# Optimization experiments

Measured on AMD Instinct MI355X. Metric: run time of the kernel, lower is better.

Reference implementation:

```python
import jax, jax.numpy as jnp
import numpy as np

N_NODES = 50000
N_EDGES = 800000
N_REL = 3
N_GRAPHS = 500
EMB = 128
IN_DIM = EMB * 3
HID = 256
N_CLASS = 10
N_SHAPE, N_COLOR, MAX_POS = 8, 8, 128


def rgcn_layer(h, src, dst, etype, W, root, b):
    """PyG RGCNConv with default aggr='mean':
    out[v] = sum_r mean_{(j->v) in E_r} h[j] @ W[r] + h[v] @ root + b
    Aggregate raw features per (dst, relation) bucket, then apply relation matmuls.
    """
    N, R = h.shape[0], W.shape[0]
    seg = dst * R + etype  # combined (node, relation) segment id
    sums = jax.ops.segment_sum(h[src], seg, num_segments=N * R)          # (N*R, d)
    cnt = jax.ops.segment_sum(jnp.ones(seg.shape, h.dtype), seg, num_segments=N * R)
    mean = (sums / jnp.maximum(cnt, 1.0)[:, None]).reshape(N, R, -1)     # (N, R, d)
    return jnp.einsum('nrd,rdh->nh', mean, W) + h @ root + b


def setup_inputs() -> dict:
    key = jax.random.key(0)
    ks = jax.random.split(key, 20)
    f32 = jnp.float32
    inp = {
        's': jax.random.randint(ks[0], (N_NODES,), 0, N_SHAPE),
        'c': jax.random.randint(ks[1], (N_NODES,), 0, N_COLOR),
        'p': jax.random.randint(ks[2], (N_NODES,), 0, MAX_POS),
        'edge_index': jax.random.randint(ks[3], (2, N_EDGES), 0, N_NODES),
        'edge_type': jax.random.randint(ks[4], (N_EDGES,), 0, N_REL),
        'batch': jnp.sort(jax.random.randint(ks[5], (N_NODES,), 0, N_GRAPHS)),
        'shape_emb': jax.random.normal(ks[6], (N_SHAPE, EMB), f32),
        'color_emb': jax.random.normal(ks[7], (N_COLOR, EMB), f32),
        'pos_emb': jax.random.normal(ks[8], (MAX_POS, EMB), f32),
        'W1': jax.random.normal(ks[9], (N_REL, IN_DIM, HID), f32) / np.sqrt(IN_DIM),
        'root1': jax.random.normal(ks[10], (IN_DIM, HID), f32) / np.sqrt(IN_DIM),
        'b1': jnp.zeros((HID,), f32),
        'W2': jax.random.normal(ks[11], (N_REL, HID, HID), f32) / np.sqrt(HID),
        'root2': jax.random.normal(ks[12], (HID, HID), f32) / np.sqrt(HID),
        'b2': jnp.zeros((HID,), f32),
        'lin_w': jax.random.normal(ks[13], (HID, N_CLASS), f32) / np.sqrt(HID),
        'lin_b': jnp.zeros((N_CLASS,), f32),
    }
    return inp


def reference(s, c, p, edge_index, edge_type, batch,
              shape_emb, color_emb, pos_emb,
              W1, root1, b1, W2, root2, b2, lin_w, lin_b):
    src, dst = edge_index[0], edge_index[1]
    h = jnp.concatenate([shape_emb[s], color_emb[c], pos_emb[p]], axis=-1)  # (N, 3*emb)
    h = jax.nn.relu(rgcn_layer(h, src, dst, edge_type, W1, root1, b1))
    h = jax.nn.relu(rgcn_layer(h, src, dst, edge_type, W2, root2, b2))
    # global_mean_pool over graphs
    gsum = jax.ops.segment_sum(h, batch, num_segments=N_GRAPHS)
    gcnt = jax.ops.segment_sum(jnp.ones((h.shape[0],), h.dtype), batch, num_segments=N_GRAPHS)
    pooled = gsum / jnp.maximum(gcnt, 1.0)[:, None]
    return pooled @ lin_w + lin_b
```

## Files before the change

kernel.cpp:

```cpp
#include <hip/hip_runtime.h>
#include <hip/hip_bf16.h>

#define NN 50000
#define NE 800000
#define NR 3
#define NG 500
#define NB (NN * NR)
#define NCLS 10
#define NCMB 8192
#define CHUNK 2048
#define NBLK ((NB + CHUNK - 1) / CHUNK)

#define P1_COMBO   196
#define P1_ZCNT    586
#define P1_ZPOOL   502
#define P1_TAB     576
#define P1_WF      1024
#define P1_TOTAL   (P1_COMBO + P1_ZCNT + P1_ZPOOL + P1_TAB + P1_WF)
#define P2_CNT     3125
#define P2_TB      768
#define P2_TOTAL   (P2_CNT + P2_TB)

#define L1_DPB     64
#define L1_HS      776
#define L1_BLOCKS  ((NN + L1_DPB - 1) / L1_DPB)

typedef __hip_bfloat16 bf16;
typedef __attribute__((ext_vector_type(8))) short short8;
typedef __attribute__((ext_vector_type(4))) short shortx4;
typedef __attribute__((ext_vector_type(4))) float floatx4;

static __device__ __forceinline__ float b2f(bf16 x) { return __bfloat162float(x); }
static __device__ __forceinline__ bf16  f2b(float x) { return __float2bfloat16(x); }
static __device__ __forceinline__ float bs2f(short x) {
    return __bfloat162float(*reinterpret_cast<const bf16*>(&x));
}
static __device__ __forceinline__ short f2bs(float x) {
    bf16 b = __float2bfloat16(x);
    return *reinterpret_cast<const short*>(&b);
}
static __device__ __forceinline__ int rfl(int x) {
    return __builtin_amdgcn_readfirstlane(x);
}

__global__ __launch_bounds__(256) void prep1(const int* __restrict__ s,
                                             const int* __restrict__ c,
                                             const int* __restrict__ p,
                                             const float* __restrict__ se,
                                             const float* __restrict__ ce,
                                             const float* __restrict__ pe,
                                             const float* __restrict__ W1,
                                             const float* __restrict__ root1,
                                             const float* __restrict__ W2,
                                             const float* __restrict__ root2,
                                             int* __restrict__ combo,
                                             unsigned* __restrict__ cnt,
                                             unsigned* __restrict__ poolz,
                                             float* __restrict__ tab,
                                             bf16* __restrict__ Wf) {
    int b = blockIdx.x, t = threadIdx.x;
    if (b < P1_COMBO) {
        int n = b * 256 + t;
        if (n < NN) combo[n] = (s[n] << 10) | (c[n] << 7) | p[n];
        return;
    }
    b -= P1_COMBO;
    if (b < P1_ZCNT) {
        int i = b * 256 + t;
        if (i < NB) cnt[i] = 0u;
        return;
    }
    b -= P1_ZCNT;
    if (b < P1_ZPOOL) {
        int i = b * 256 + t;
        if (i < NG * 256 + NG) poolz[i] = 0u;
        return;
    }
    b -= P1_ZPOOL;
    if (b < P1_TAB) {
        int r = b / 144, row = b % 144;
        const float* A; int segk;
        if (row < 8)       { A = se + row * 128;        segk = 0; }
        else if (row < 16) { A = ce + (row - 8) * 128;  segk = 128; }
        else               { A = pe + (row - 16) * 128; segk = 256; }
        const float* W = (r < 3) ? (W1 + (size_t)r * 384 * 256) : root1;
        float acc = 0.f;
        for (int k = 0; k < 128; ++k)
            acc += A[k] * W[(size_t)(segk + k) * 256 + t];
        tab[((size_t)r * 144 + row) * 256 + t] = acc;
        return;
    }
    b -= P1_TAB;
    {
        int idx = b * 256 + t;
        int j     = idx & 7;
        int lane  = (idx >> 3) & 63;
        int ni    = (idx >> 9) & 3;
        int chunk = (idx >> 11) & 31;
        int colblk = idx >> 16;
        int col = colblk * 64 + ni * 16 + (lane & 15);
        int k   = chunk * 32 + (lane >> 4) * 8 + j;
        float v = (k < 768) ? W2[((size_t)(k >> 8) * 256 + (k & 255)) * 256 + col]
                            : root2[(size_t)(k - 768) * 256 + col];
        Wf[idx] = f2b(v);
    }
}

__global__ __launch_bounds__(256) void prep2(const int* __restrict__ ei,
                                             const int* __restrict__ et,
                                             int* __restrict__ cnt,
                                             const float* __restrict__ tab,
                                             const float* __restrict__ b1,
                                             bf16* __restrict__ tb2) {
    int b = blockIdx.x, t = threadIdx.x;
    if (b < P2_CNT) {
        int e = b * 256 + t;
        if (e < NE) atomicAdd(&cnt[ei[NE + e] * NR + et[e]], 1);
        return;
    }
    b -= P2_CNT;
    if (b < 256) {
        int r = b >> 6, sc = b & 63, si = sc >> 3, ci = sc & 7;
        float v = tab[((size_t)r * 144 + si) * 256 + t]
                + tab[((size_t)r * 144 + 8 + ci) * 256 + t];
        if (r == 3) v += b1[t];
        tb2[(size_t)b * 256 + t] = f2b(v);
    } else {
        int bb = b - 256;
        int r = bb >> 7, pi = bb & 127;
        tb2[(size_t)(256 + bb) * 256 + t] =
            f2b(tab[((size_t)r * 144 + 16 + pi) * 256 + t]);
    }
}

__global__ __launch_bounds__(256) void prep3(const bf16* __restrict__ tb2,
                                             bf16* __restrict__ tbf) {
    int idx = blockIdx.x * 256 + threadIdx.x;
    int j = idx & 7, lane = (idx >> 3) & 63, ni = (idx >> 9) & 3;
    int rest = idx >> 11;
    int chunk = rest % 24, colblk = rest / 24;
    int col = colblk * 64 + ni * 16 + (lane & 15);
    int k   = chunk * 32 + (lane >> 4) * 8 + j;
    tbf[idx] = tb2[(size_t)k * 256 + col];
}

__global__ __launch_bounds__(256) void scan_block_sums(const int* __restrict__ cnt,
                                                       int* __restrict__ bsum) {
    __shared__ int sm[256];
    int b = blockIdx.x, t = threadIdx.x;
    int base = b * CHUNK + t * 8, s = 0;
#pragma unroll
    for (int j = 0; j < 8; ++j) { int i = base + j; if (i < NB) s += cnt[i]; }
    sm[t] = s; __syncthreads();
    for (int st = 128; st; st >>= 1) { if (t < st) sm[t] += sm[t + st]; __syncthreads(); }
    if (!t) bsum[b] = sm[0];
}

__global__ __launch_bounds__(256) void scan_write(const int* __restrict__ cnt,
                                                  const int* __restrict__ bsum,
                                                  int* __restrict__ off,
                                                  int* __restrict__ cursor) {
    int b = blockIdx.x, t = threadIdx.x;
    int bbase = 0;
    for (int i = 0; i < b; ++i) bbase += bsum[i];
    if (b == 0 && t == 0) {
        int tot = 0;
        for (int i = 0; i < NBLK; ++i) tot += bsum[i];
        off[NB] = tot;
    }
    int base = b * CHUNK + t * 8;
    int v[8], ts = 0;
#pragma unroll
    for (int j = 0; j < 8; ++j) { int i = base + j; v[j] = (i < NB) ? cnt[i] : 0; ts += v[j]; }
    int lane = t & 63, wv = t >> 6;
    int incl = ts;
    for (int d = 1; d < 64; d <<= 1) {
        int o = __shfl_up(incl, d, 64);
        if (lane >= d) incl += o;
    }
    __shared__ int wsum[4];
    if (lane == 63) wsum[wv] = incl;
    __syncthreads();
    int wbase = 0;
    for (int w = 0; w < wv; ++w) wbase += wsum[w];
    int run = bbase + wbase + incl - ts;
#pragma unroll
    for (int j = 0; j < 8; ++j) {
        int i = base + j;
        if (i < NB) { off[i] = run; cursor[i] = run; }
        run += v[j];
    }
}

__global__ __launch_bounds__(256) void scatter_edges(const int* __restrict__ ei,
                                                     const int* __restrict__ et,
                                                     const int* __restrict__ combo,
                                                     int* __restrict__ cursor,
                                                     unsigned* __restrict__ esc) {
    int e = blockIdx.x * 256 + threadIdx.x;
    if (e >= NE) return;
    int b = ei[NE + e] * NR + et[e];
    int pos = atomicAdd(&cursor[b], 1);
    int s = ei[e];
    esc[pos] = ((unsigned)s << 13) | (unsigned)combo[s];
}

__global__ __launch_bounds__(256) void l1_hist(const int* __restrict__ off,
                                               const unsigned* __restrict__ esc,
                                               const int* __restrict__ combo,
                                               const bf16* __restrict__ tbf,
                                               bf16* __restrict__ h1) {
    __shared__ __align__(16) unsigned char HIST[L1_DPB * L1_HS];
    __shared__ int SOFF[193];
    __shared__ float INV[L1_DPB][4];
    const int t = threadIdx.x;
    const int dst0 = blockIdx.x * L1_DPB;

    for (int i = t; i < (L1_DPB * L1_HS) / 4; i += 256)
        ((unsigned*)HIST)[i] = 0u;
    for (int i = t; i < 193; i += 256)
        SOFF[i] = off[min(dst0 * NR + i, NB)];
    __syncthreads();

    if (t < L1_DPB) {
        int base = 3 * t;
#pragma unroll
        for (int r = 0; r < 3; ++r) {
            int c = SOFF[base + r + 1] - SOFF[base + r];
            INV[t][r] = (c > 0) ? 1.f / (float)c : 0.f;
        }
        INV[t][3] = 1.f;
        if (dst0 + t < NN) {
            int c = combo[dst0 + t];
            HIST[t * L1_HS + 192 + (c >> 7)] = 1;
            HIST[t * L1_HS + 640 + (c & 127)] = 1;
        }
    }
    int E0 = SOFF[0], E1 = SOFF[192];
    for (int e = E0 + t; e < E1; e += 256) {
        unsigned ev = esc[e];
        int lo = 0, hi = 191;
#pragma unroll 1
        while (lo < hi) {
            int mid = (lo + hi + 1) >> 1;
            if (SOFF[mid] <= e) lo = mid; else hi = mid - 1;
        }
        int dr = lo / 3, rel = lo - dr * 3;
        int sc = (int)((ev & 8191u) >> 7), p = (int)(ev & 127u);
        int a1 = dr * L1_HS + rel * 64 + sc;
        int a2 = dr * L1_HS + 256 + rel * 128 + p;
        atomicAdd((unsigned*)&HIST[a1 & ~3], 1u << (8 * (a1 & 3)));
        atomicAdd((unsigned*)&HIST[a2 & ~3], 1u << (8 * (a2 & 3)));
    }
    __syncthreads();

    const int wave = t >> 6, lane = t & 63;
    const int quad = lane >> 4, l16 = lane & 15;
    const short8* bb = (const short8*)tbf + (size_t)wave * 24 * 4 * 64 + lane;
    floatx4 acc[4][4] = {};
#pragma unroll 4
    for (int ch = 0; ch < 24; ++ch) {
        short8 bf_[4];
        const short8* bp = bb + (size_t)ch * 4 * 64;
#pragma unroll
        for (int ni = 0; ni < 4; ++ni) bf_[ni] = bp[ni * 64];
        int kb = ch * 32 + quad * 8;
        int iv = (kb < 256) ? (kb >> 6) : ((kb - 256) >> 7);
#pragma unroll
        for (int mi = 0; mi < 4; ++mi) {
            int row = mi * 16 + l16;
            unsigned hx = *(const unsigned*)&HIST[row * L1_HS + kb];
            unsigned hy = *(const unsigned*)&HIST[row * L1_HS + kb + 4];
            float w = INV[row][iv];
            short8 af;
            af[0] = f2bs((float)(hx & 0xffu) * w);
            af[1] = f2bs((float)((hx >> 8) & 0xffu) * w);
            af[2] = f2bs((float)((hx >> 16) & 0xffu) * w);
            af[3] = f2bs((float)(hx >> 24) * w);
            af[4] = f2bs((float)(hy & 0xffu) * w);
            af[5] = f2bs((float)((hy >> 8) & 0xffu) * w);
            af[6] = f2bs((float)((hy >> 16) & 0xffu) * w);
            af[7] = f2bs((float)(hy >> 24) * w);
#pragma unroll
            for (int ni = 0; ni < 4; ++ni)
                acc[mi][ni] = __builtin_amdgcn_mfma_f32_16x16x32_bf16(af, bf_[ni], acc[mi][ni], 0, 0, 0);
        }
    }

    __syncthreads();
    short* st = (short*)HIST;
#pragma unroll
    for (int mi = 0; mi < 4; ++mi)
#pragma unroll
        for (int ni = 0; ni < 4; ++ni)
#pragma unroll
            for (int ii = 0; ii < 4; ++ii) {
                int row = mi * 16 + quad * 4 + ii;
                int col = wave * 64 + ni * 16 + l16;
                st[row * 264 + col] = f2bs(fmaxf(acc[mi][ni][ii], 0.f));
            }
    __syncthreads();
    int row = t >> 2, cb = (t & 3) * 64;
    if (dst0 + row < NN) {
#pragma unroll
        for (int j = 0; j < 8; ++j)
            *(short8*)(h1 + (size_t)(dst0 + row) * 256 + cb + j * 8) =
                *(const short8*)&st[row * 264 + cb + j * 8];
    }
}

__global__ __launch_bounds__(256, 4) void agg_all(const int* __restrict__ off,
                                                  const unsigned* __restrict__ esc,
                                                  const bf16* __restrict__ h1,
                                                  bf16* __restrict__ hagg) {
    int wave = threadIdx.x >> 6, lane = threadIdx.x & 63;
    int dst = blockIdx.x * 4 + wave;
    if (dst >= NN) return;
    int l4 = lane * 4;
    int b0 = dst * NR;
    int o0 = rfl(off[b0]),     o1 = rfl(off[b0 + 1]),
        o2 = rfl(off[b0 + 2]), o3 = rfl(off[b0 + 3]);
    int nmin = min(o1 - o0, min(o2 - o1, o3 - o2));
    float s0[4] = {}, s1[4] = {}, s2[4] = {};
    int k = 0;
    for (; k + 2 <= nmin; k += 2) {
        unsigned ea0 = esc[o0 + k], ea1 = esc[o0 + k + 1];
        unsigned eb0 = esc[o1 + k], eb1 = esc[o1 + k + 1];
        unsigned ec0 = esc[o2 + k], ec1 = esc[o2 + k + 1];
        shortx4 va0 = *(const shortx4*)(h1 + (size_t)(ea0 >> 13) * 256 + l4);
        shortx4 va1 = *(const shortx4*)(h1 + (size_t)(ea1 >> 13) * 256 + l4);
        shortx4 vb0 = *(const shortx4*)(h1 + (size_t)(eb0 >> 13) * 256 + l4);
        shortx4 vb1 = *(const shortx4*)(h1 + (size_t)(eb1 >> 13) * 256 + l4);
        shortx4 vc0 = *(const shortx4*)(h1 + (size_t)(ec0 >> 13) * 256 + l4);
        shortx4 vc1 = *(const shortx4*)(h1 + (size_t)(ec1 >> 13) * 256 + l4);
#pragma unroll
        for (int i = 0; i < 4; ++i) {
            s0[i] += bs2f(va0[i]) + bs2f(va1[i]);
            s1[i] += bs2f(vb0[i]) + bs2f(vb1[i]);
            s2[i] += bs2f(vc0[i]) + bs2f(vc1[i]);
        }
    }
    for (int j = o0 + k; j < o1; j += 2) {
        bool g = j + 1 < o1;
        unsigned e0 = esc[j], e1 = esc[g ? j + 1 : j];
        shortx4 v0 = *(const shortx4*)(h1 + (size_t)(e0 >> 13) * 256 + l4);
        shortx4 v1 = *(const shortx4*)(h1 + (size_t)(e1 >> 13) * 256 + l4);
        float m = g ? 1.f : 0.f;
#pragma unroll
        for (int i = 0; i < 4; ++i) s0[i] += bs2f(v0[i]) + bs2f(v1[i]) * m;
    }
    for (int j = o1 + k; j < o2; j += 2) {
        bool g = j + 1 < o2;
        unsigned e0 = esc[j], e1 = esc[g ? j + 1 : j];
        shortx4 v0 = *(const shortx4*)(h1 + (size_t)(e0 >> 13) * 256 + l4);
        shortx4 v1 = *(const shortx4*)(h1 + (size_t)(e1 >> 13) * 256 + l4);
        float m = g ? 1.f : 0.f;
#pragma unroll
        for (int i = 0; i < 4; ++i) s1[i] += bs2f(v0[i]) + bs2f(v1[i]) * m;
    }
    for (int j = o2 + k; j < o3; j += 2) {
        bool g = j + 1 < o3;
        unsigned e0 = esc[j], e1 = esc[g ? j + 1 : j];
        shortx4 v0 = *(const shortx4*)(h1 + (size_t)(e0 >> 13) * 256 + l4);
        shortx4 v1 = *(const shortx4*)(h1 + (size_t)(e1 >> 13) * 256 + l4);
        float m = g ? 1.f : 0.f;
#pragma unroll
        for (int i = 0; i < 4; ++i) s2[i] += bs2f(v0[i]) + bs2f(v1[i]) * m;
    }
    float inv0 = (o1 > o0) ? 1.f / (float)(o1 - o0) : 0.f;
    float inv1 = (o2 > o1) ? 1.f / (float)(o2 - o1) : 0.f;
    float inv2 = (o3 > o2) ? 1.f / (float)(o3 - o2) : 0.f;
    shortx4 w0, w1, w2;
#pragma unroll
    for (int i = 0; i < 4; ++i) {
        w0[i] = f2bs(s0[i] * inv0);
        w1[i] = f2bs(s1[i] * inv1);
        w2[i] = f2bs(s2[i] * inv2);
    }
    bf16* hd = hagg + (size_t)dst * 768 + l4;
    *(shortx4*)(hd)       = w0;
    *(shortx4*)(hd + 256) = w1;
    *(shortx4*)(hd + 512) = w2;
}

__global__ __launch_bounds__(256) void gemm_cat(const bf16* __restrict__ hagg,
                                                const bf16* __restrict__ h1,
                                                const bf16* __restrict__ Wf,
                                                const float* __restrict__ bias,
                                                const int* __restrict__ batch,
                                                float* __restrict__ pool,
                                                float* __restrict__ gcnt) {
    __shared__ short lds[4][2][32 * 40];
    const int t = threadIdx.x;
    const int wave = t >> 6, lane = t & 63;
    const int quad = lane >> 4, l16 = lane & 15;
    const int row0 = blockIdx.x * 32;
    const int colblk = wave;
    const int rsub = lane >> 2;
    const int ksub = (lane & 3) * 8;
    short* A0 = lds[wave][0];
    short* A1 = lds[wave][1];

    const int r0 = min(row0 + rsub, NN - 1);
    const int r1 = min(row0 + 16 + rsub, NN - 1);
    const bf16* gA0 = hagg + (size_t)r0 * 768 + ksub;
    const bf16* gA1 = hagg + (size_t)r1 * 768 + ksub;
    const bf16* gH0 = h1 + (size_t)r0 * 256 + ksub;
    const bf16* gH1 = h1 + (size_t)r1 * 256 + ksub;
    const short8* bbase = (const short8*)Wf + (size_t)colblk * 32 * 4 * 64 + lane;

    auto loadA2 = [&](int k0, short8& a0, short8& a1) {
        if (k0 < 768) { a0 = *(const short8*)(gA0 + k0); a1 = *(const short8*)(gA1 + k0); }
        else          { a0 = *(const short8*)(gH0 + k0 - 768); a1 = *(const short8*)(gH1 + k0 - 768); }
    };
    auto loadB = [&](int chunk, short8* bf4) {
        const short8* bp = bbase + (size_t)chunk * 4 * 64;
#pragma unroll
        for (int ni = 0; ni < 4; ++ni) bf4[ni] = bp[ni * 64];
    };

    floatx4 acc[2][4] = {};
    short8 aE0, aE1, bE[4];
    short8 aO0, aO1, bO[4];
    loadA2(0, aE0, aE1);  loadB(0, bE);
    loadA2(32, aO0, aO1); loadB(1, bO);

#pragma unroll
    for (int i = 0; i < 32; i += 2) {
        *(short8*)&A0[rsub * 40 + ksub] = aE0;
        *(short8*)&A0[(16 + rsub) * 40 + ksub] = aE1;
        {
            short8 af0 = *(const short8*)&A0[l16 * 40 + quad * 8];
            short8 af1 = *(const short8*)&A0[(16 + l16) * 40 + quad * 8];
#pragma unroll
            for (int ni = 0; ni < 4; ++ni) {
                acc[0][ni] = __builtin_amdgcn_mfma_f32_16x16x32_bf16(af0, bE[ni], acc[0][ni], 0, 0, 0);
                acc[1][ni] = __builtin_amdgcn_mfma_f32_16x16x32_bf16(af1, bE[ni], acc[1][ni], 0, 0, 0);
            }
        }
        if (i + 2 < 32) { loadA2((i + 2) * 32, aE0, aE1); loadB(i + 2, bE); }
        *(short8*)&A1[rsub * 40 + ksub] = aO0;
        *(short8*)&A1[(16 + rsub) * 40 + ksub] = aO1;
        {
            short8 af0 = *(const short8*)&A1[l16 * 40 + quad * 8];
            short8 af1 = *(const short8*)&A1[(16 + l16) * 40 + quad * 8];
#pragma unroll
            for (int ni = 0; ni < 4; ++ni) {
                acc[0][ni] = __builtin_amdgcn_mfma_f32_16x16x32_bf16(af0, bO[ni], acc[0][ni], 0, 0, 0);
                acc[1][ni] = __builtin_amdgcn_mfma_f32_16x16x32_bf16(af1, bO[ni], acc[1][ni], 0, 0, 0);
            }
        }
        if (i + 3 < 32) { loadA2((i + 3) * 32, aO0, aO1); loadB(i + 3, bO); }
    }

    __syncthreads();
    short* st = &lds[0][0][0];
#pragma unroll
    for (int mi = 0; mi < 2; ++mi) {
#pragma unroll
        for (int ni = 0; ni < 4; ++ni) {
            int n = colblk * 64 + ni * 16 + l16;
            float bn = bias[n];
#pragma unroll
            for (int ii = 0; ii < 4; ++ii) {
                int lrow = mi * 16 + quad * 4 + ii;
                float v = (row0 + lrow < NN) ? fmaxf(acc[mi][ni][ii] + bn, 0.f) : 0.f;
                st[lrow * 260 + n] = f2bs(v);
            }
        }
    }
    __syncthreads();
    int nrows = NN - row0; if (nrows > 32) nrows = 32;
    int curg = batch[row0];
    float a = 0.f, cntf = 0.f;
    for (int rr = 0; rr < nrows; ++rr) {
        int g = batch[row0 + rr];
        if (g != curg) {
            atomicAdd(&pool[(size_t)curg * 256 + t], a);
            if (t == 0) atomicAdd(&gcnt[curg], cntf);
            a = 0.f; cntf = 0.f; curg = g;
        }
        a += bs2f(st[rr * 260 + t]);
        cntf += 1.f;
    }
    atomicAdd(&pool[(size_t)curg * 256 + t], a);
    if (t == 0) atomicAdd(&gcnt[curg], cntf);
}

__global__ __launch_bounds__(256) void final_head(const float* __restrict__ pool,
                                                  const float* __restrict__ gcnt,
                                                  const float* __restrict__ lin_w,
                                                  const float* __restrict__ lin_b,
                                                  float* __restrict__ out) {
    __shared__ float sm[256];
    int g = blockIdx.x, t = threadIdx.x;
    float inv = 1.0f / fmaxf(gcnt[g], 1.0f);
    sm[t] = pool[(size_t)g * 256 + t] * inv;
    __syncthreads();
    if (t < NCLS) {
        float s = lin_b[t];
        for (int d = 0; d < 256; ++d) s += sm[d] * lin_w[d * NCLS + t];
        out[g * NCLS + t] = s;
    }
}

extern "C" void kernel_launch(void* const* d_in, const int* in_sizes, int n_in,
                              void* d_out, int out_size, void* d_ws, size_t ws_size,
                              hipStream_t stream) {
    const int*   s_idx = (const int*)d_in[0];
    const int*   c_idx = (const int*)d_in[1];
    const int*   p_idx = (const int*)d_in[2];
    const int*   ei    = (const int*)d_in[3];
    const int*   et    = (const int*)d_in[4];
    const int*   batch = (const int*)d_in[5];
    const float* se    = (const float*)d_in[6];
    const float* ce    = (const float*)d_in[7];
    const float* pe    = (const float*)d_in[8];
    const float* W1    = (const float*)d_in[9];
    const float* root1 = (const float*)d_in[10];
    const float* b1    = (const float*)d_in[11];
    const float* W2    = (const float*)d_in[12];
    const float* root2 = (const float*)d_in[13];
    const float* b2    = (const float*)d_in[14];
    const float* lin_w = (const float*)d_in[15];
    const float* lin_b = (const float*)d_in[16];
    float* out = (float*)d_out;

    char* w = (char*)d_ws;
    size_t o = 0;
    auto alloc = [&](size_t bytes) -> void* {
        o = (o + 15) & ~(size_t)15;
        void* ptr = w + o;
        o += bytes;
        return ptr;
    };
    bf16*     hagg   = (bf16*)    alloc((size_t)NN * 768 * 2);
    bf16*     h1     = (bf16*)    alloc((size_t)NN * 256 * 2);
    bf16*     tb2    = (bf16*)    alloc((size_t)768 * 256 * 2);
    bf16*     tbf    = (bf16*)    alloc((size_t)768 * 256 * 2);
    int*      combo  = (int*)     alloc((size_t)NN * 4);
    unsigned* esc    = (unsigned*)alloc((size_t)NE * 4);
    int*      cnt    = (int*)     alloc((size_t)NB * 4);
    int*      off    = (int*)     alloc((size_t)(NB + 1) * 4);
    int*      cursor = (int*)     alloc((size_t)NB * 4);
    int*      bsum   = (int*)     alloc((size_t)NBLK * 4);
    float*    tab    = (float*)   alloc((size_t)4 * 144 * 256 * 4);
    bf16*     Wf     = (bf16*)    alloc((size_t)256 * 1024 * 2);
    float*    pool   = (float*)   alloc((size_t)NG * 256 * 4);
    float*    gcnt   = (float*)   alloc((size_t)NG * 4);
    (void)ws_size;

    prep1<<<P1_TOTAL, 256, 0, stream>>>(s_idx, c_idx, p_idx, se, ce, pe,
                                        W1, root1, W2, root2,
                                        combo, (unsigned*)cnt, (unsigned*)pool, tab, Wf);
    prep2<<<P2_TOTAL, 256, 0, stream>>>(ei, et, cnt, tab, b1, tb2);
    prep3<<<768, 256, 0, stream>>>(tb2, tbf);
    scan_block_sums<<<NBLK, 256, 0, stream>>>(cnt, bsum);
    scan_write<<<NBLK, 256, 0, stream>>>(cnt, bsum, off, cursor);
    scatter_edges<<<(NE + 255) / 256, 256, 0, stream>>>(ei, et, combo, cursor, esc);
    l1_hist<<<L1_BLOCKS, 256, 0, stream>>>(off, esc, combo, tbf, h1);
    agg_all<<<(NN + 3) / 4, 256, 0, stream>>>(off, esc, h1, hagg);
    gemm_cat<<<(NN + 31) / 32, 256, 0, stream>>>(hagg, h1, Wf, b2, batch, pool, gcnt);
    final_head<<<NG, 256, 0, stream>>>(pool, gcnt, lin_w, lin_b, out);
}
```

Baseline: 360.3 us.

## Double gemm_cat row tile to 64 rows per block for more B reuse

The layer-2 GEMM kernel now computes 64 output rows per block instead of 32, giving each wave four 16-row MFMA groups. Each loaded B fragment (the fused weight matrix) is reused across twice as many rows, halving weight traffic per output and halving the number of blocks and pooling atomics. In exchange it doubles the accumulator registers and LDS per block, which may lower occupancy, and the grid shrinks to about 782 blocks. The epilogue LDS stride is adjusted to 264 so the larger staging tile fits.

```diff
diff --git a/kernel.cpp b/kernel.cpp
--- a/kernel.cpp
+++ b/kernel.cpp
@@ -390,28 +390,35 @@
                                                 const int* __restrict__ batch,
                                                 float* __restrict__ pool,
                                                 float* __restrict__ gcnt) {
-    __shared__ short lds[4][2][32 * 40];
+    __shared__ short lds[4][2][64 * 40];
     const int t = threadIdx.x;
     const int wave = t >> 6, lane = t & 63;
     const int quad = lane >> 4, l16 = lane & 15;
-    const int row0 = blockIdx.x * 32;
+    const int row0 = blockIdx.x * 64;
     const int colblk = wave;
     const int rsub = lane >> 2;
     const int ksub = (lane & 3) * 8;
     short* A0 = lds[wave][0];
     short* A1 = lds[wave][1];
 
-    const int r0 = min(row0 + rsub, NN - 1);
-    const int r1 = min(row0 + 16 + rsub, NN - 1);
-    const bf16* gA0 = hagg + (size_t)r0 * 768 + ksub;
-    const bf16* gA1 = hagg + (size_t)r1 * 768 + ksub;
-    const bf16* gH0 = h1 + (size_t)r0 * 256 + ksub;
-    const bf16* gH1 = h1 + (size_t)r1 * 256 + ksub;
+    int rr_[4];
+    const bf16 *gA[4], *gH[4];
+#pragma unroll
+    for (int g = 0; g < 4; ++g) {
+        rr_[g] = min(row0 + g * 16 + rsub, NN - 1);
+        gA[g] = hagg + (size_t)rr_[g] * 768 + ksub;
+        gH[g] = h1 + (size_t)rr_[g] * 256 + ksub;
+    }
     const short8* bbase = (const short8*)Wf + (size_t)colblk * 32 * 4 * 64 + lane;
 
-    auto loadA2 = [&](int k0, short8& a0, short8& a1) {
-        if (k0 < 768) { a0 = *(const short8*)(gA0 + k0); a1 = *(const short8*)(gA1 + k0); }
-        else          { a0 = *(const short8*)(gH0 + k0 - 768); a1 = *(const short8*)(gH1 + k0 - 768); }
+    auto loadA4 = [&](int k0, short8* a) {
+        if (k0 < 768) {
+#pragma unroll
+            for (int g = 0; g < 4; ++g) a[g] = *(const short8*)(gA[g] + k0);
+        } else {
+#pragma unroll
+            for (int g = 0; g < 4; ++g) a[g] = *(const short8*)(gH[g] + k0 - 768);
+        }
     };
     auto loadB = [&](int chunk, short8* bf4) {
         const short8* bp = bbase + (size_t)chunk * 4 * 64;
@@ -419,44 +426,46 @@
         for (int ni = 0; ni < 4; ++ni) bf4[ni] = bp[ni * 64];
     };
 
-    floatx4 acc[2][4] = {};
-    short8 aE0, aE1, bE[4];
-    short8 aO0, aO1, bO[4];
-    loadA2(0, aE0, aE1);  loadB(0, bE);
-    loadA2(32, aO0, aO1); loadB(1, bO);
+    floatx4 acc[4][4] = {};
+    short8 aE[4], bE[4];
+    short8 aO[4], bO[4];
+    loadA4(0, aE);  loadB(0, bE);
+    loadA4(32, aO); loadB(1, bO);
 
 #pragma unroll
     for (int i = 0; i < 32; i += 2) {
-        *(short8*)&A0[rsub * 40 + ksub] = aE0;
-        *(short8*)&A0[(16 + rsub) * 40 + ksub] = aE1;
+#pragma unroll
+        for (int g = 0; g < 4; ++g)
+            *(short8*)&A0[(g * 16 + rsub) * 40 + ksub] = aE[g];
         {
-            short8 af0 = *(const short8*)&A0[l16 * 40 + quad * 8];
-            short8 af1 = *(const short8*)&A0[(16 + l16) * 40 + quad * 8];
-#pragma unroll
-            for (int ni = 0; ni < 4; ++ni) {
-                acc[0][ni] = __builtin_amdgcn_mfma_f32_16x16x32_bf16(af0, bE[ni], acc[0][ni], 0, 0, 0);
-                acc[1][ni] = __builtin_amdgcn_mfma_f32_16x16x32_bf16(af1, bE[ni], acc[1][ni], 0, 0, 0);
+#pragma unroll
+            for (int g = 0; g < 4; ++g) {
+                short8 af = *(const short8*)&A0[(g * 16 + l16) * 40 + quad * 8];
+#pragma unroll
+                for (int ni = 0; ni < 4; ++ni)
+                    acc[g][ni] = __builtin_amdgcn_mfma_f32_16x16x32_bf16(af, bE[ni], acc[g][ni], 0, 0, 0);
             }
         }
-        if (i + 2 < 32) { loadA2((i + 2) * 32, aE0, aE1); loadB(i + 2, bE); }
-        *(short8*)&A1[rsub * 40 + ksub] = aO0;
-        *(short8*)&A1[(16 + rsub) * 40 + ksub] = aO1;
+        if (i + 2 < 32) { loadA4((i + 2) * 32, aE); loadB(i + 2, bE); }
+#pragma unroll
+        for (int g = 0; g < 4; ++g)
+            *(short8*)&A1[(g * 16 + rsub) * 40 + ksub] = aO[g];
         {
-            short8 af0 = *(const short8*)&A1[l16 * 40 + quad * 8];
-            short8 af1 = *(const short8*)&A1[(16 + l16) * 40 + quad * 8];
-#pragma unroll
-            for (int ni = 0; ni < 4; ++ni) {
-                acc[0][ni] = __builtin_amdgcn_mfma_f32_16x16x32_bf16(af0, bO[ni], acc[0][ni], 0, 0, 0);
-                acc[1][ni] = __builtin_amdgcn_mfma_f32_16x16x32_bf16(af1, bO[ni], acc[1][ni], 0, 0, 0);
+#pragma unroll
+            for (int g = 0; g < 4; ++g) {
+                short8 af = *(const short8*)&A1[(g * 16 + l16) * 40 + quad * 8];
+#pragma unroll
+                for (int ni = 0; ni < 4; ++ni)
+                    acc[g][ni] = __builtin_amdgcn_mfma_f32_16x16x32_bf16(af, bO[ni], acc[g][ni], 0, 0, 0);
             }
         }
-        if (i + 3 < 32) { loadA2((i + 3) * 32, aO0, aO1); loadB(i + 3, bO); }
+        if (i + 3 < 32) { loadA4((i + 3) * 32, aO); loadB(i + 3, bO); }
     }
 
     __syncthreads();
     short* st = &lds[0][0][0];
 #pragma unroll
-    for (int mi = 0; mi < 2; ++mi) {
+    for (int mi = 0; mi < 4; ++mi) {
 #pragma unroll
         for (int ni = 0; ni < 4; ++ni) {
             int n = colblk * 64 + ni * 16 + l16;
@@ -465,12 +474,12 @@
             for (int ii = 0; ii < 4; ++ii) {
                 int lrow = mi * 16 + quad * 4 + ii;
                 float v = (row0 + lrow < NN) ? fmaxf(acc[mi][ni][ii] + bn, 0.f) : 0.f;
-                st[lrow * 260 + n] = f2bs(v);
+                st[lrow * 264 + n] = f2bs(v);
             }
         }
     }
     __syncthreads();
-    int nrows = NN - row0; if (nrows > 32) nrows = 32;
+    int nrows = NN - row0; if (nrows > 64) nrows = 64;
     int curg = batch[row0];
     float a = 0.f, cntf = 0.f;
     for (int rr = 0; rr < nrows; ++rr) {
@@ -480,7 +489,7 @@
             if (t == 0) atomicAdd(&gcnt[curg], cntf);
             a = 0.f; cntf = 0.f; curg = g;
         }
-        a += bs2f(st[rr * 260 + t]);
+        a += bs2f(st[rr * 264 + t]);
         cntf += 1.f;
     }
     atomicAdd(&pool[(size_t)curg * 256 + t], a);
@@ -560,6 +569,6 @@
     scatter_edges<<<(NE + 255) / 256, 256, 0, stream>>>(ei, et, combo, cursor, esc);
     l1_hist<<<L1_BLOCKS, 256, 0, stream>>>(off, esc, combo, tbf, h1);
     agg_all<<<(NN + 3) / 4, 256, 0, stream>>>(off, esc, h1, hagg);
-    gemm_cat<<<(NN + 31) / 32, 256, 0, stream>>>(hagg, h1, Wf, b2, batch, pool, gcnt);
+    gemm_cat<<<(NN + 63) / 64, 256, 0, stream>>>(hagg, h1, Wf, b2, batch, pool, gcnt);
     final_head<<<NG, 256, 0, stream>>>(pool, gcnt, lin_w, lin_b, out);
 }
```

Result: no change. 357.7 us (-0.7%).
